# Kernel optimization log

Hardware: AMD Instinct MI355X
Metric: run time of the kernel (lower is better)

## Reference

```python
import jax, jax.numpy as jnp
import numpy as np

B, T, V, H, D = 32, 2048, 8, 5, 128  # batch, time, n_vars, history_len, d_model


def _init_w(k, shape, fan_in):
    return jax.random.normal(k, shape, jnp.float32) * (1.0 / np.sqrt(fan_in))


def setup_inputs() -> dict:
    key = jax.random.key(0)
    ks = jax.random.split(key, 8)
    return {
        "x": jax.random.normal(ks[0], (B, T, V), jnp.float32),
        "history": jax.random.normal(ks[1], (B, T, V * H), jnp.float32),
        # context_encoder: Linear(V*H -> D), ReLU, Linear(D -> V*V)
        "ce_w1": _init_w(ks[2], (D, V * H), V * H),
        "ce_b1": jnp.zeros((D,), jnp.float32),
        "ce_w2": _init_w(ks[3], (V * V, D), D),
        "ce_b2": jnp.zeros((V * V,), jnp.float32),
        # projector: Linear(1 -> D), ReLU, Linear(D -> D)
        "p_w1": _init_w(ks[4], (D, 1), 1),
        "p_b1": jnp.zeros((D,), jnp.float32),
        "p_w2": _init_w(ks[5], (D, D), D),
        "p_b2": jnp.zeros((D,), jnp.float32),
        # Wq / Wk: Linear(D -> D, bias=False)
        "wq": _init_w(ks[6], (D, D), D),
        "wk": _init_w(ks[7], (D, D), D),
    }


def reference(x, history, ce_w1, ce_b1, ce_w2, ce_b2,
              p_w1, p_b1, p_w2, p_b2, wq, wk):
    b, t, v = x.shape
    d = wq.shape[0]
    # gate: sigmoid(context_encoder(history)) reshaped to [B,T,V,V]
    h = jax.nn.relu(history @ ce_w1.T + ce_b1)                      # [B,T,D]
    gate = jax.nn.sigmoid((h @ ce_w2.T + ce_b2).reshape(b, t, v, v))
    # projector applied per scalar: Linear(1->D) == x[...,None] * w1_col + b1
    feat = jax.nn.relu(x[..., None] * p_w1[:, 0] + p_b1)            # [B,T,V,D]
    feat = feat @ p_w2.T + p_b2                                     # [B,T,V,D]
    q = feat @ wq.T                                                 # [B,T,V,D]
    k = feat @ wk.T                                                 # [B,T,V,D]
    scores = jnp.einsum('btid,btjd->btij', q, k) / jnp.sqrt(jnp.asarray(d, feat.dtype))
    A = jnp.tanh(scores) * gate                                     # [B,T,V,V]
    pred = jnp.einsum('btij,btj->bti', A, x)                        # [B,T,V]
    return pred, A
```

## Files before the change

### kernel.cpp

```cpp
#include <hip/hip_runtime.h>
#include <hip/hip_bf16.h>
#include <stdint.h>

#define Dm 128
#define BTOT (32 * 2048)

typedef short s16x8 __attribute__((ext_vector_type(8)));
typedef float f32x4 __attribute__((ext_vector_type(4)));

__device__ float g_Wq[Dm * Dm];
__device__ float g_Wk[Dm * Dm];
__device__ float g_bq[Dm], g_bk[Dm];
__device__ float g_u[Dm], g_w[Dm], g_c[1];
__device__ __align__(16) unsigned short g_AllFrag[32768];

__device__ __forceinline__ float fast_sigmoid(float x) { return 1.0f / (1.0f + __expf(-x)); }
__device__ __forceinline__ float fast_tanh(float x) { return 1.0f - 2.0f / (__expf(2.0f * x) + 1.0f); }

__device__ __forceinline__ unsigned short f2bf(float f) {
    unsigned u = __float_as_uint(f);
    u += 0x7fffu + ((u >> 16) & 1u);
    return (unsigned short)(u >> 16);
}

__device__ __forceinline__ unsigned pk2(float lo, float hi) {
    unsigned short ua = __builtin_bit_cast(unsigned short, (__bf16)lo);
    unsigned short ub = __builtin_bit_cast(unsigned short, (__bf16)hi);
    return (unsigned)ua | ((unsigned)ub << 16);
}

__device__ __forceinline__ s16x8 mk8(unsigned a, unsigned b, unsigned c, unsigned d) {
    union { unsigned u[4]; s16x8 v; } t;
    t.u[0] = a; t.u[1] = b; t.u[2] = c; t.u[3] = d;
    return t.v;
}

__device__ __forceinline__ void compute_rpf(float xv, int g,
                                            const float* __restrict__ p_w1,
                                            const float* __restrict__ p_b1,
                                            s16x8* rpf, float& sj_out) {
    float sj = 0.f;
#pragma unroll
    for (int kc = 0; kc < 4; ++kc) {
        unsigned wds[4];
#pragma unroll
        for (int jh = 0; jh < 2; ++jh) {
            const int d4 = kc * 32 + 4 * g + 16 * jh;
            f32x4 w1v = *(const f32x4*)&p_w1[d4];
            f32x4 b1v = *(const f32x4*)&p_b1[d4];
            f32x4 wvv = *(const f32x4*)&g_w[d4];
            float v[4];
#pragma unroll
            for (int jj = 0; jj < 4; ++jj) {
                float val = fmaxf(fmaf(xv, w1v[jj], b1v[jj]), 0.f);
                sj = fmaf(wvv[jj], val, sj);
                v[jj] = val;
            }
            wds[jh * 2 + 0] = pk2(v[0], v[1]);
            wds[jh * 2 + 1] = pk2(v[2], v[3]);
        }
        rpf[kc] = mk8(wds[0], wds[1], wds[2], wds[3]);
    }
    sj += __shfl_xor(sj, 16);
    sj += __shfl_xor(sj, 32);
    sj_out = sj;
}

__global__ __launch_bounds__(128) void k_pre1(const float* __restrict__ wq,
                                              const float* __restrict__ wk,
                                              const float* __restrict__ pw2,
                                              const float* __restrict__ pb2,
                                              const float* __restrict__ ce_w1,
                                              const float* __restrict__ ce_b1,
                                              const float* __restrict__ ce_w2) {
    const int b = blockIdx.x, t = threadIdx.x;
    if (b < 128) {
        const int g = b, d = t;
        float aq = 0.f, ak = 0.f;
        for (int f = 0; f < Dm; ++f) {
            float pv = pw2[f * Dm + d];
            aq = fmaf(wq[g * Dm + f], pv, aq);
            ak = fmaf(wk[g * Dm + f], pv, ak);
        }
        g_Wq[g * Dm + d] = aq;
        g_Wk[g * Dm + d] = ak;
        if (d == 0) {
            float bq = 0.f, bk = 0.f;
            for (int f = 0; f < Dm; ++f) {
                bq = fmaf(wq[g * Dm + f], pb2[f], bq);
                bk = fmaf(wk[g * Dm + f], pb2[f], bk);
            }
            g_bq[g] = bq;
            g_bk[g] = bk;
        }
    } else if (b < 136) {
        const int s = (b - 128) * 128 + t;
        const int l = s & 63, slot = s >> 6;
        const int rt = slot >> 1, kc = slot & 1;
        const int row = rt * 16 + (l & 15), gg = l >> 4;
#pragma unroll
        for (int j = 0; j < 8; ++j) {
            int k = kc * 32 + 4 * gg + (j & 3) + 16 * (j >> 2);
            float v = (k < 40) ? ce_w1[row * 40 + k] : ((k == 40) ? ce_b1[row] : 0.f);
            g_AllFrag[24576 + s * 8 + j] = f2bf(v);
        }
    } else {
        const int s = (b - 136) * 128 + t;
        const int l = s & 63, slot = s >> 6;
        const int rt2 = slot >> 2, kc = slot & 3;
        const int o = rt2 * 16 + (l & 15), gg = l >> 4;
#pragma unroll
        for (int j = 0; j < 8; ++j) {
            int k = kc * 32 + 4 * gg + (j & 3) + 16 * (j >> 2);
            g_AllFrag[16384 + s * 8 + j] = f2bf(ce_w2[o * Dm + k]);
        }
    }
}

__global__ __launch_bounds__(128) void k_pre2() {
    const int b = blockIdx.x, tid = threadIdx.x;
    if (b < 128) {
        const int slot = b >> 2, jj = b & 3;
        const int kc = slot & 3, rt = slot >> 2;
        const int l = tid & 63, jh = tid >> 6;
        const int row = rt * 16 + (l & 15), g = l >> 4;
        const int e = kc * 32 + 4 * g + jj + 16 * jh;
        float acc = 0.f;
        for (int gg = 0; gg < Dm; ++gg)
            acc = fmaf(g_Wq[gg * Dm + row], g_Wk[gg * Dm + e], acc);
        g_AllFrag[(slot * 64 + l) * 8 + 4 * jh + jj] = f2bf(acc);
    } else {
        const int d = tid;
        float ua = 0.f, wa = 0.f;
        for (int g = 0; g < Dm; ++g) {
            ua = fmaf(g_Wq[g * Dm + d], g_bk[g], ua);
            wa = fmaf(g_Wk[g * Dm + d], g_bq[g], wa);
        }
        g_u[d] = ua;
        g_w[d] = wa;
        if (d == 0) {
            float c = 0.f;
            for (int g = 0; g < Dm; ++g) c = fmaf(g_bq[g], g_bk[g], c);
            g_c[0] = c;
        }
    }
}

__global__ __launch_bounds__(256) void k_fused(const float* __restrict__ x,
                                               const float* __restrict__ hist,
                                               const float* __restrict__ ce_b2,
                                               const float* __restrict__ p_w1,
                                               const float* __restrict__ p_b1,
                                               float* __restrict__ pred_out,
                                               float* __restrict__ A_out) {
    __shared__ __align__(16) unsigned short lds_m[16384];
    __shared__ __align__(16) unsigned short lds_hB[2048];
    __shared__ __align__(16) char lds_hg[16 * 41 * 4];
    float* lds_hist = (float*)lds_hg;
    unsigned* lds_gateP = (unsigned*)lds_hg;

    const int tid = threadIdx.x;
    const int wv = tid >> 6;
    const int l = tid & 63;
    const int g = l >> 4, c16 = l & 15;
    const long base = (long)blockIdx.x * 16;

    {
        const char* gsrc = (const char*)g_AllFrag + (size_t)wv * 8192 + (size_t)l * 16;
        char* ldst = (char*)lds_m + wv * 8192;
#pragma unroll
        for (int q = 0; q < 8; ++q)
            __builtin_amdgcn_global_load_lds(
                (const __attribute__((address_space(1))) unsigned int*)(gsrc + q * 1024),
                (__attribute__((address_space(3))) unsigned int*)(ldst + q * 1024), 16, 0, 0);
    }
    {
        const float* hsrc = hist + base * 40;
        lds_hist[(tid / 40) * 41 + (tid % 40)] = hsrc[tid];
        int i2 = tid + 256;
        lds_hist[(i2 / 40) * 41 + (i2 % 40)] = hsrc[i2];
        if (tid < 128) {
            int i3 = tid + 512;
            lds_hist[(i3 / 40) * 41 + (i3 % 40)] = hsrc[i3];
        }
    }
    s16x8 w1fA[2][2];
#pragma unroll
    for (int rr = 0; rr < 2; ++rr)
#pragma unroll
        for (int kc = 0; kc < 2; ++kc)
            w1fA[rr][kc] = *(const s16x8*)&g_AllFrag[24576 + (((2 * wv + rr) * 2 + kc) * 64 + l) * 8];
    s16x8 w2fA[4];
#pragma unroll
    for (int kc = 0; kc < 4; ++kc)
        w2fA[kc] = *(const s16x8*)&g_AllFrag[16384 + ((wv * 4 + kc) * 64 + l) * 8];
    f32x4 b2v = *(const f32x4*)&ce_b2[16 * wv + 4 * g];

    const int np = c16 >> 3, i_me = c16 & 7;
    const float xv0 = x[(base + wv * 4 + 0 + np) * 8 + i_me];
    const float xv1 = x[(base + wv * 4 + 2 + np) * 8 + i_me];
    s16x8 rpf0[4], rpf1[4];
    float sj0, sj1;
    compute_rpf(xv0, g, p_w1, p_b1, rpf0, sj0);
    compute_rpf(xv1, g, p_w1, p_b1, rpf1, sj1);
    const float cc = g_c[0];

    __syncthreads();

    const float* hl = lds_hist + c16 * 41;
    s16x8 histB[2];
    histB[0] = mk8(pk2(hl[4 * g + 0], hl[4 * g + 1]),
                   pk2(hl[4 * g + 2], hl[4 * g + 3]),
                   pk2(hl[16 + 4 * g + 0], hl[16 + 4 * g + 1]),
                   pk2(hl[16 + 4 * g + 2], hl[16 + 4 * g + 3]));
    {
        float v[4];
#pragma unroll
        for (int jj = 0; jj < 4; ++jj) {
            int k = 32 + 4 * g + jj;
            int kk = (k < 40) ? k : 0;
            float t = hl[kk];
            t = (k < 40) ? t : 0.f;
            v[jj] = (k == 40) ? 1.f : t;
        }
        histB[1] = mk8(pk2(v[0], v[1]), pk2(v[2], v[3]), 0u, 0u);
    }

#pragma unroll
    for (int rr = 0; rr < 2; ++rr) {
        f32x4 hC = (f32x4){0.f, 0.f, 0.f, 0.f};
        hC = __builtin_amdgcn_mfma_f32_16x16x32_bf16(w1fA[rr][0], histB[0], hC, 0, 0, 0);
        hC = __builtin_amdgcn_mfma_f32_16x16x32_bf16(w1fA[rr][1], histB[1], hC, 0, 0, 0);
        unsigned* dst = (unsigned*)&lds_hB[(wv * 64 + l) * 8 + rr * 4];
        dst[0] = pk2(fmaxf(hC[0], 0.f), fmaxf(hC[1], 0.f));
        dst[1] = pk2(fmaxf(hC[2], 0.f), fmaxf(hC[3], 0.f));
    }

    __syncthreads();

    {
        s16x8 gB[4];
#pragma unroll
        for (int kc = 0; kc < 4; ++kc)
            gB[kc] = *(const s16x8*)&lds_hB[(kc * 64 + l) * 8];
        f32x4 gC = b2v;
#pragma unroll
        for (int kc = 0; kc < 4; ++kc)
            gC = __builtin_amdgcn_mfma_f32_16x16x32_bf16(w2fA[kc], gB[kc], gC, 0, 0, 0);
        unsigned* gp = lds_gateP + c16 * 33 + 8 * wv + 2 * g;
        gp[0] = pk2(fast_sigmoid(gC[0]), fast_sigmoid(gC[1]));
        gp[1] = pk2(fast_sigmoid(gC[2]), fast_sigmoid(gC[3]));
    }

    f32x4 Sacc0 = (f32x4){0.f, 0.f, 0.f, 0.f};
    f32x4 Sacc1 = (f32x4){0.f, 0.f, 0.f, 0.f};
#pragma unroll
    for (int rt = 0; rt < 4; ++rt) {
        const int r0 = 2 * rt, r1 = 2 * rt + 1;
        f32x4 uv0 = *(const f32x4*)&g_u[16 * r0 + 4 * g];
        f32x4 uv1 = *(const f32x4*)&g_u[16 * r1 + 4 * g];
        f32x4 Ya0 = uv0, Yb0 = uv1;
        f32x4 Ya1 = uv0, Yb1 = uv1;
#pragma unroll
        for (int kc = 0; kc < 4; ++kc) {
            s16x8 af0 = *(const s16x8*)&lds_m[((r0 * 4 + kc) * 64 + l) * 8];
            s16x8 af1 = *(const s16x8*)&lds_m[((r1 * 4 + kc) * 64 + l) * 8];
            Ya0 = __builtin_amdgcn_mfma_f32_16x16x32_bf16(af0, rpf0[kc], Ya0, 0, 0, 0);
            Ya1 = __builtin_amdgcn_mfma_f32_16x16x32_bf16(af0, rpf1[kc], Ya1, 0, 0, 0);
            Yb0 = __builtin_amdgcn_mfma_f32_16x16x32_bf16(af1, rpf0[kc], Yb0, 0, 0, 0);
            Yb1 = __builtin_amdgcn_mfma_f32_16x16x32_bf16(af1, rpf1[kc], Yb1, 0, 0, 0);
        }
        s16x8 yf0 = mk8(pk2(Ya0[0], Ya0[1]), pk2(Ya0[2], Ya0[3]),
                        pk2(Yb0[0], Yb0[1]), pk2(Yb0[2], Yb0[3]));
        s16x8 yf1 = mk8(pk2(Ya1[0], Ya1[1]), pk2(Ya1[2], Ya1[3]),
                        pk2(Yb1[0], Yb1[1]), pk2(Yb1[2], Yb1[3]));
        Sacc0 = __builtin_amdgcn_mfma_f32_16x16x32_bf16(rpf0[rt], yf0, Sacc0, 0, 0, 0);
        Sacc1 = __builtin_amdgcn_mfma_f32_16x16x32_bf16(rpf1[rt], yf1, Sacc1, 0, 0, 0);
    }

    __syncthreads();

    const int jv = c16 & 7;
    const bool diag = ((g >> 1) == np);
    auto do_epi = [&](const f32x4& Sacc, float sjv, float xvv, int s) {
        const int bp = wv * 4 + s * 2 + np;
        const long bt = base + bp;
        float Av[4], pr[4];
#pragma unroll
        for (int q = 0; q < 4; ++q) {
            float sc = (Sacc[q] + sjv + cc) * 0.08838834764831845f;
            unsigned wg = lds_gateP[bp * 33 + (4 * (g & 1) + q) * 4 + (jv >> 1)];
            float gv = __uint_as_float((jv & 1) ? (wg & 0xffff0000u) : (wg << 16));
            Av[q] = fast_tanh(sc) * gv;
            pr[q] = Av[q] * xvv;
            pr[q] += __shfl_xor(pr[q], 1);
            pr[q] += __shfl_xor(pr[q], 2);
            pr[q] += __shfl_xor(pr[q], 4);
        }
        if (diag) {
            float* Ap = A_out + bt * 64 + jv;
#pragma unroll
            for (int q = 0; q < 4; ++q) Ap[((g & 1) * 4 + q) * 8] = Av[q];
            if (jv == 0) {
                float* Pp = pred_out + bt * 8 + (g & 1) * 4;
#pragma unroll
                for (int q = 0; q < 4; ++q) Pp[q] = pr[q];
            }
        }
    };
    do_epi(Sacc0, sj0, xv0, 0);
    do_epi(Sacc1, sj1, xv1, 1);
}

extern "C" void kernel_launch(void* const* d_in, const int* in_sizes, int n_in,
                              void* d_out, int out_size, void* d_ws, size_t ws_size,
                              hipStream_t stream) {
    const float* x = (const float*)d_in[0];
    const float* hist = (const float*)d_in[1];
    const float* ce_w1 = (const float*)d_in[2];
    const float* ce_b1 = (const float*)d_in[3];
    const float* ce_w2 = (const float*)d_in[4];
    const float* ce_b2 = (const float*)d_in[5];
    const float* p_w1 = (const float*)d_in[6];
    const float* p_b1 = (const float*)d_in[7];
    const float* p_w2 = (const float*)d_in[8];
    const float* p_b2 = (const float*)d_in[9];
    const float* wq = (const float*)d_in[10];
    const float* wk = (const float*)d_in[11];

    float* pred_out = (float*)d_out;
    float* A_out = pred_out + (size_t)BTOT * 8;

    k_pre1<<<144, 128, 0, stream>>>(wq, wk, p_w2, p_b2, ce_w1, ce_b1, ce_w2);
    k_pre2<<<129, 128, 0, stream>>>();
    k_fused<<<BTOT / 16, 256, 0, stream>>>(x, hist, ce_b2, p_w1, p_b1, pred_out, A_out);
}
```

Measured before the change: 68.07 us.

## Process 32 timesteps per block to amortize weight fragment loads

```diff
diff --git a/kernel.cpp b/kernel.cpp
--- a/kernel.cpp
+++ b/kernel.cpp
@@ -154,8 +154,8 @@
                                                float* __restrict__ pred_out,
                                                float* __restrict__ A_out) {
     __shared__ __align__(16) unsigned short lds_m[16384];
-    __shared__ __align__(16) unsigned short lds_hB[2048];
-    __shared__ __align__(16) char lds_hg[16 * 41 * 4];
+    __shared__ __align__(16) unsigned short lds_hB[4096];
+    __shared__ __align__(16) char lds_hg[32 * 41 * 4];
     float* lds_hist = (float*)lds_hg;
     unsigned* lds_gateP = (unsigned*)lds_hg;
 
@@ -163,7 +163,7 @@
     const int wv = tid >> 6;
     const int l = tid & 63;
     const int g = l >> 4, c16 = l & 15;
-    const long base = (long)blockIdx.x * 16;
+    const long base = (long)blockIdx.x * 32;
 
     {
         const char* gsrc = (const char*)g_AllFrag + (size_t)wv * 8192 + (size_t)l * 16;
@@ -176,12 +176,10 @@
     }
     {
         const float* hsrc = hist + base * 40;
-        lds_hist[(tid / 40) * 41 + (tid % 40)] = hsrc[tid];
-        int i2 = tid + 256;
-        lds_hist[(i2 / 40) * 41 + (i2 % 40)] = hsrc[i2];
-        if (tid < 128) {
-            int i3 = tid + 512;
-            lds_hist[(i3 / 40) * 41 + (i3 % 40)] = hsrc[i3];
+#pragma unroll
+        for (int q = 0; q < 5; ++q) {
+            int idx = tid + q * 256;
+            lds_hist[(idx / 40) * 41 + (idx % 40)] = hsrc[idx];
         }
     }
     s16x8 w1fA[2][2];
@@ -197,23 +195,25 @@
     f32x4 b2v = *(const f32x4*)&ce_b2[16 * wv + 4 * g];
 
     const int np = c16 >> 3, i_me = c16 & 7;
-    const float xv0 = x[(base + wv * 4 + 0 + np) * 8 + i_me];
-    const float xv1 = x[(base + wv * 4 + 2 + np) * 8 + i_me];
-    s16x8 rpf0[4], rpf1[4];
-    float sj0, sj1;
-    compute_rpf(xv0, g, p_w1, p_b1, rpf0, sj0);
-    compute_rpf(xv1, g, p_w1, p_b1, rpf1, sj1);
+    float xv[4], sj[4];
+    s16x8 rpf[4][4];
+#pragma unroll
+    for (int s = 0; s < 4; ++s) {
+        xv[s] = x[(base + wv * 8 + s * 2 + np) * 8 + i_me];
+        compute_rpf(xv[s], g, p_w1, p_b1, rpf[s], sj[s]);
+    }
     const float cc = g_c[0];
 
     __syncthreads();
 
-    const float* hl = lds_hist + c16 * 41;
-    s16x8 histB[2];
-    histB[0] = mk8(pk2(hl[4 * g + 0], hl[4 * g + 1]),
-                   pk2(hl[4 * g + 2], hl[4 * g + 3]),
-                   pk2(hl[16 + 4 * g + 0], hl[16 + 4 * g + 1]),
-                   pk2(hl[16 + 4 * g + 2], hl[16 + 4 * g + 3]));
-    {
+    s16x8 histB[2][2];
+#pragma unroll
+    for (int cg = 0; cg < 2; ++cg) {
+        const float* hl = lds_hist + (cg * 16 + c16) * 41;
+        histB[cg][0] = mk8(pk2(hl[4 * g + 0], hl[4 * g + 1]),
+                           pk2(hl[4 * g + 2], hl[4 * g + 3]),
+                           pk2(hl[16 + 4 * g + 0], hl[16 + 4 * g + 1]),
+                           pk2(hl[16 + 4 * g + 2], hl[16 + 4 * g + 3]));
         float v[4];
 #pragma unroll
         for (int jj = 0; jj < 4; ++jj) {
@@ -223,76 +223,83 @@
             t = (k < 40) ? t : 0.f;
             v[jj] = (k == 40) ? 1.f : t;
         }
-        histB[1] = mk8(pk2(v[0], v[1]), pk2(v[2], v[3]), 0u, 0u);
-    }
-
-#pragma unroll
-    for (int rr = 0; rr < 2; ++rr) {
-        f32x4 hC = (f32x4){0.f, 0.f, 0.f, 0.f};
-        hC = __builtin_amdgcn_mfma_f32_16x16x32_bf16(w1fA[rr][0], histB[0], hC, 0, 0, 0);
-        hC = __builtin_amdgcn_mfma_f32_16x16x32_bf16(w1fA[rr][1], histB[1], hC, 0, 0, 0);
-        unsigned* dst = (unsigned*)&lds_hB[(wv * 64 + l) * 8 + rr * 4];
-        dst[0] = pk2(fmaxf(hC[0], 0.f), fmaxf(hC[1], 0.f));
-        dst[1] = pk2(fmaxf(hC[2], 0.f), fmaxf(hC[3], 0.f));
-    }
+        histB[cg][1] = mk8(pk2(v[0], v[1]), pk2(v[2], v[3]), 0u, 0u);
+    }
+
+#pragma unroll
+    for (int rr = 0; rr < 2; ++rr)
+#pragma unroll
+        for (int cg = 0; cg < 2; ++cg) {
+            f32x4 hC = (f32x4){0.f, 0.f, 0.f, 0.f};
+            hC = __builtin_amdgcn_mfma_f32_16x16x32_bf16(w1fA[rr][0], histB[cg][0], hC, 0, 0, 0);
+            hC = __builtin_amdgcn_mfma_f32_16x16x32_bf16(w1fA[rr][1], histB[cg][1], hC, 0, 0, 0);
+            unsigned* dst = (unsigned*)&lds_hB[cg * 2048 + (wv * 64 + l) * 8 + rr * 4];
+            dst[0] = pk2(fmaxf(hC[0], 0.f), fmaxf(hC[1], 0.f));
+            dst[1] = pk2(fmaxf(hC[2], 0.f), fmaxf(hC[3], 0.f));
+        }
 
     __syncthreads();
 
-    {
+#pragma unroll
+    for (int cg = 0; cg < 2; ++cg) {
         s16x8 gB[4];
 #pragma unroll
         for (int kc = 0; kc < 4; ++kc)
-            gB[kc] = *(const s16x8*)&lds_hB[(kc * 64 + l) * 8];
+            gB[kc] = *(const s16x8*)&lds_hB[cg * 2048 + (kc * 64 + l) * 8];
         f32x4 gC = b2v;
 #pragma unroll
         for (int kc = 0; kc < 4; ++kc)
             gC = __builtin_amdgcn_mfma_f32_16x16x32_bf16(w2fA[kc], gB[kc], gC, 0, 0, 0);
-        unsigned* gp = lds_gateP + c16 * 33 + 8 * wv + 2 * g;
+        unsigned* gp = lds_gateP + (cg * 16 + c16) * 33 + 8 * wv + 2 * g;
         gp[0] = pk2(fast_sigmoid(gC[0]), fast_sigmoid(gC[1]));
         gp[1] = pk2(fast_sigmoid(gC[2]), fast_sigmoid(gC[3]));
     }
 
-    f32x4 Sacc0 = (f32x4){0.f, 0.f, 0.f, 0.f};
-    f32x4 Sacc1 = (f32x4){0.f, 0.f, 0.f, 0.f};
+    f32x4 Sacc[4];
+#pragma unroll
+    for (int s = 0; s < 4; ++s) Sacc[s] = (f32x4){0.f, 0.f, 0.f, 0.f};
 #pragma unroll
     for (int rt = 0; rt < 4; ++rt) {
         const int r0 = 2 * rt, r1 = 2 * rt + 1;
         f32x4 uv0 = *(const f32x4*)&g_u[16 * r0 + 4 * g];
         f32x4 uv1 = *(const f32x4*)&g_u[16 * r1 + 4 * g];
-        f32x4 Ya0 = uv0, Yb0 = uv1;
-        f32x4 Ya1 = uv0, Yb1 = uv1;
+        f32x4 Ya[4], Yb[4];
+#pragma unroll
+        for (int s = 0; s < 4; ++s) { Ya[s] = uv0; Yb[s] = uv1; }
 #pragma unroll
         for (int kc = 0; kc < 4; ++kc) {
             s16x8 af0 = *(const s16x8*)&lds_m[((r0 * 4 + kc) * 64 + l) * 8];
             s16x8 af1 = *(const s16x8*)&lds_m[((r1 * 4 + kc) * 64 + l) * 8];
-            Ya0 = __builtin_amdgcn_mfma_f32_16x16x32_bf16(af0, rpf0[kc], Ya0, 0, 0, 0);
-            Ya1 = __builtin_amdgcn_mfma_f32_16x16x32_bf16(af0, rpf1[kc], Ya1, 0, 0, 0);
-            Yb0 = __builtin_amdgcn_mfma_f32_16x16x32_bf16(af1, rpf0[kc], Yb0, 0, 0, 0);
-            Yb1 = __builtin_amdgcn_mfma_f32_16x16x32_bf16(af1, rpf1[kc], Yb1, 0, 0, 0);
-        }
-        s16x8 yf0 = mk8(pk2(Ya0[0], Ya0[1]), pk2(Ya0[2], Ya0[3]),
-                        pk2(Yb0[0], Yb0[1]), pk2(Yb0[2], Yb0[3]));
-        s16x8 yf1 = mk8(pk2(Ya1[0], Ya1[1]), pk2(Ya1[2], Ya1[3]),
-                        pk2(Yb1[0], Yb1[1]), pk2(Yb1[2], Yb1[3]));
-        Sacc0 = __builtin_amdgcn_mfma_f32_16x16x32_bf16(rpf0[rt], yf0, Sacc0, 0, 0, 0);
-        Sacc1 = __builtin_amdgcn_mfma_f32_16x16x32_bf16(rpf1[rt], yf1, Sacc1, 0, 0, 0);
+#pragma unroll
+            for (int s = 0; s < 4; ++s) {
+                Ya[s] = __builtin_amdgcn_mfma_f32_16x16x32_bf16(af0, rpf[s][kc], Ya[s], 0, 0, 0);
+                Yb[s] = __builtin_amdgcn_mfma_f32_16x16x32_bf16(af1, rpf[s][kc], Yb[s], 0, 0, 0);
+            }
+        }
+#pragma unroll
+        for (int s = 0; s < 4; ++s) {
+            s16x8 yf = mk8(pk2(Ya[s][0], Ya[s][1]), pk2(Ya[s][2], Ya[s][3]),
+                           pk2(Yb[s][0], Yb[s][1]), pk2(Yb[s][2], Yb[s][3]));
+            Sacc[s] = __builtin_amdgcn_mfma_f32_16x16x32_bf16(rpf[s][rt], yf, Sacc[s], 0, 0, 0);
+        }
     }
 
     __syncthreads();
 
     const int jv = c16 & 7;
     const bool diag = ((g >> 1) == np);
-    auto do_epi = [&](const f32x4& Sacc, float sjv, float xvv, int s) {
-        const int bp = wv * 4 + s * 2 + np;
+#pragma unroll
+    for (int s = 0; s < 4; ++s) {
+        const int bp = wv * 8 + s * 2 + np;
         const long bt = base + bp;
         float Av[4], pr[4];
 #pragma unroll
         for (int q = 0; q < 4; ++q) {
-            float sc = (Sacc[q] + sjv + cc) * 0.08838834764831845f;
+            float sc = (Sacc[s][q] + sj[s] + cc) * 0.08838834764831845f;
             unsigned wg = lds_gateP[bp * 33 + (4 * (g & 1) + q) * 4 + (jv >> 1)];
             float gv = __uint_as_float((jv & 1) ? (wg & 0xffff0000u) : (wg << 16));
             Av[q] = fast_tanh(sc) * gv;
-            pr[q] = Av[q] * xvv;
+            pr[q] = Av[q] * xv[s];
             pr[q] += __shfl_xor(pr[q], 1);
             pr[q] += __shfl_xor(pr[q], 2);
             pr[q] += __shfl_xor(pr[q], 4);
@@ -307,9 +314,7 @@
                 for (int q = 0; q < 4; ++q) Pp[q] = pr[q];
             }
         }
-    };
-    do_epi(Sacc0, sj0, xv0, 0);
-    do_epi(Sacc1, sj1, xv1, 1);
+    }
 }
 
 extern "C" void kernel_launch(void* const* d_in, const int* in_sizes, int n_in,
@@ -333,5 +338,5 @@
 
     k_pre1<<<144, 128, 0, stream>>>(wq, wk, p_w2, p_b2, ce_w1, ce_b1, ce_w2);
     k_pre2<<<129, 128, 0, stream>>>();
-    k_fused<<<BTOT / 16, 256, 0, stream>>>(x, hist, ce_b2, p_w1, p_b1, pred_out, A_out);
-}
+    k_fused<<<BTOT / 32, 256, 0, stream>>>(x, hist, ce_b2, p_w1, p_b1, pred_out, A_out);
+}
```

New measurement: 80.81 us. 1.19x slower.
